# Kernel optimization log

Hardware: AMD Instinct MI355X
Metric: run time of the kernel (lower is better)

The kernel has to match this reference:

```python
import jax, jax.numpy as jnp
import numpy as np

DIM_X = 256
DIM_E = 256
SCALE = (DIM_X + DIM_E) ** -0.5


def setup_inputs() -> dict:
    key = jax.random.key(0)
    k1, k2, k3, k4 = jax.random.split(key, 4)
    b, n = 8, 2048
    d = DIM_X + DIM_E
    x = jax.random.normal(k1, (b, n, DIM_X), dtype=jnp.float32)
    e = jax.random.normal(k2, (n, DIM_E), dtype=jnp.float32)
    # nn.Linear(d, d, bias=False) weights, torch layout (out, in): y = x @ W.T
    Wq = jax.random.normal(k3, (d, d), dtype=jnp.float32) * 0.02
    Wk = jax.random.normal(k4, (d, d), dtype=jnp.float32) * 0.02
    return {"x": x, "e": e, "Wq": Wq, "Wk": Wk}


def reference(x, e, Wq, Wk):
    b, n, t = x.shape
    # e repeated across batch, concatenated with x along feature dim
    e_b = jnp.broadcast_to(e[None], (b, n, e.shape[-1]))
    x_e = jnp.concatenate([x, e_b], axis=-1)            # (b, n, dX+dE)
    queries = x_e @ Wq.T                                 # (b, n, d)
    keys = x_e @ Wk.T                                    # (b, n, d)
    # raw bilinear scores, no softmax; dropout=0 (eval) is identity
    attn = jnp.einsum('bnd,bmd->bnm', queries, keys) * SCALE
    out = jnp.einsum('bnm,bmt->bnt', attn, x)            # v = x
    return out
```

## Files before the change

kernel.cpp:

```cpp
#include <hip/hip_runtime.h>
#include <hip/hip_bf16.h>

#define DIM_X 256
#define DIM_E 256
#define DD    512
#define NB    8
#define NN    2048
#define SCALE 0.044194173824159216f

typedef __attribute__((ext_vector_type(8))) __bf16 bf16x8;
typedef __attribute__((ext_vector_type(4))) float  f32x4;
using bf16 = __hip_bfloat16;

__device__ __forceinline__ unsigned short f2bf(float f) {
  union { __hip_bfloat16 h; unsigned short u; } c;
  c.h = __float2bfloat16(f);
  return c.u;
}

__device__ __forceinline__ void async_lds16(const void* g, void* l) {
  using u32_as3 = __attribute__((address_space(3))) unsigned int;
  using u32_as1 = const __attribute__((address_space(1))) unsigned int;
  __builtin_amdgcn_global_load_lds(
      reinterpret_cast<u32_as1*>(reinterpret_cast<unsigned long long>(g)),
      reinterpret_cast<u32_as3*>(static_cast<unsigned int>(
          reinterpret_cast<unsigned long long>(l))),
      16, 0, 0);
}

__global__ __launch_bounds__(256, 4) void pack_k(
    const float* __restrict__ x, const float* __restrict__ e,
    const float* __restrict__ Wq, const float* __restrict__ Wk, bf16* xb,
    bf16* VT, bf16* eb, bf16* ET, bf16* WqT, bf16* WkT) {
  __shared__ float tile[32][33];
  const int tid  = threadIdx.x;
  const int lrow = tid >> 3;
  const int lc4  = (tid & 7) * 4;
  for (int j = blockIdx.x; j < 5120; j += 1024) {
    const float* src; int ld;
    bf16 *dS = nullptr, *dT; int ldS = 0, ldT;
    if (j < 4096) {
      int b = j >> 9, r = (j >> 3) & 63, c = j & 7;
      src = x + ((long)b * NN + r * 32) * DIM_X + c * 32; ld = DIM_X;
      dS = xb + ((long)b * NN + r * 32) * DIM_X + c * 32; ldS = DIM_X;
      dT = VT + ((long)b * DIM_X + c * 32) * NN + r * 32; ldT = NN;
    } else if (j < 4608) {
      int i = j - 4096, r = i >> 3, c = i & 7;
      src = e + ((long)r * 32) * DIM_E + c * 32; ld = DIM_E;
      dS = eb + ((long)r * 32) * DIM_E + c * 32; ldS = DIM_E;
      dT = ET + ((long)c * 32) * NN + r * 32; ldT = NN;
    } else if (j < 4864) {
      int i = j - 4608, r = i >> 4, c = i & 15;
      src = Wq + ((long)r * 32) * DD + c * 32; ld = DD;
      dT = WqT + ((long)c * 32) * DD + r * 32; ldT = DD;
    } else {
      int i = j - 4864, r = i >> 4, c = i & 15;
      src = Wk + ((long)r * 32) * DD + c * 32; ld = DD;
      dT = WkT + ((long)c * 32) * DD + r * 32; ldT = DD;
    }
    float4 v = *(const float4*)(src + (long)lrow * ld + lc4);
    if (dS) {
      ushort4 o;
      o.x = f2bf(v.x); o.y = f2bf(v.y); o.z = f2bf(v.z); o.w = f2bf(v.w);
      *(ushort4*)((unsigned short*)dS + (long)lrow * ldS + lc4) = o;
    }
    tile[lrow][lc4 + 0] = v.x; tile[lrow][lc4 + 1] = v.y;
    tile[lrow][lc4 + 2] = v.z; tile[lrow][lc4 + 3] = v.w;
    __syncthreads();
    {
      ushort4 o;
      o.x = f2bf(tile[lc4 + 0][lrow]);
      o.y = f2bf(tile[lc4 + 1][lrow]);
      o.z = f2bf(tile[lc4 + 2][lrow]);
      o.w = f2bf(tile[lc4 + 3][lrow]);
      *(ushort4*)((unsigned short*)dT + (long)lrow * ldT + lc4) = o;
    }
    __syncthreads();
  }
}

template <int BM, int BN, int BKt, bool OUT_BF16>
__device__ void gemm_tile(const bf16* __restrict__ A0,
                          const bf16* __restrict__ A1,
                          const bf16* __restrict__ B, void* __restrict__ Cv,
                          int K, int lda, int ldb, int ldc, float alpha,
                          char* smem) {
  constexpr int CPT = BKt / 8;
  constexpr int KS  = BKt / 32;
  constexpr int WTM = BM / 2, WTN = BN / 2;
  constexpr int IM = WTM / 16, IN = WTN / 16;
  constexpr int CA = BM * CPT, CB = BN * CPT;
  bf16* sA = (bf16*)smem;
  bf16* sB = (bf16*)(smem + (size_t)BM * BKt * 2);

  const int tid  = threadIdx.x;
  const int lane = tid & 63;
  const int wave = tid >> 6;
  const int lm   = lane & 15;
  const int quad = lane >> 4;
  const int wm   = (wave >> 1) * WTM;
  const int wn   = (wave & 1) * WTN;

  f32x4 acc[IM][IN];
#pragma unroll
  for (int i = 0; i < IM; i++)
#pragma unroll
    for (int j = 0; j < IN; j++) acc[i][j] = (f32x4){0.f, 0.f, 0.f, 0.f};

  for (int k0 = 0; k0 < K; k0 += BKt) {
    const bf16* Ak = A0; int kk = k0;
    if (A1 != nullptr && k0 >= 256) { Ak = A1; kk = k0 - 256; }
#pragma unroll
    for (int c = tid; c < CA; c += 256) {
      int row = c / CPT;
      int cb  = (c % CPT) ^ (row % CPT);
      async_lds16(Ak + (long)row * lda + kk + cb * 8, sA + (size_t)c * 8);
    }
#pragma unroll
    for (int c = tid; c < CB; c += 256) {
      int row = c / CPT;
      int cb  = (c % CPT) ^ (row % CPT);
      async_lds16(B + (long)row * ldb + k0 + cb * 8, sB + (size_t)c * 8);
    }
    __syncthreads();

    bf16x8 af[KS][IM], bfr[KS][IN];
#pragma unroll
    for (int s = 0; s < KS; s++) {
#pragma unroll
      for (int i = 0; i < IM; i++) {
        int r = wm + i * 16 + lm;
        af[s][i] = *(const bf16x8*)&sA[r * BKt +
                                       (((s * 4 + quad) ^ (r % CPT)) * 8)];
      }
#pragma unroll
      for (int j = 0; j < IN; j++) {
        int r = wn + j * 16 + lm;
        bfr[s][j] = *(const bf16x8*)&sB[r * BKt +
                                        (((s * 4 + quad) ^ (r % CPT)) * 8)];
      }
    }
#pragma unroll
    for (int s = 0; s < KS; s++)
#pragma unroll
      for (int i = 0; i < IM; i++)
#pragma unroll
        for (int j = 0; j < IN; j++)
          acc[i][j] = __builtin_amdgcn_mfma_f32_16x16x32_bf16(
              af[s][i], bfr[s][j], acc[i][j], 0, 0, 0);
    __syncthreads();
  }

  const int baseRow = wm + quad * 4;
  const int baseCol = wn + lm;
  if (OUT_BF16) {
    bf16* Cb = (bf16*)Cv;
#pragma unroll
    for (int i = 0; i < IM; i++)
#pragma unroll
      for (int r = 0; r < 4; r++) {
        int row = baseRow + i * 16 + r;
#pragma unroll
        for (int j = 0; j < IN; j++)
          Cb[(long)row * ldc + baseCol + j * 16] =
              __float2bfloat16(acc[i][j][r] * alpha);
      }
  } else {
    float* Cf = (float*)Cv;
#pragma unroll
    for (int i = 0; i < IM; i++)
#pragma unroll
      for (int r = 0; r < 4; r++) {
        int row = baseRow + i * 16 + r;
#pragma unroll
        for (int j = 0; j < IN; j++)
          Cf[(long)row * ldc + baseCol + j * 16] = acc[i][j][r] * alpha;
      }
  }
}

__global__ __launch_bounds__(256, 4) void phase1_k(const bf16* VT,
                                                   const bf16* ET,
                                                   const bf16* WqT,
                                                   const bf16* WkT, bf16* M,
                                                   bf16* W2T) {
  __shared__ __align__(16) char smem[32768];
  const int bx = blockIdx.x;
  if (bx < 512) {
    int b = bx & 7, r = (bx >> 3) & 7, c = bx >> 6;
    const bf16* A = VT + (long)b * DIM_X * NN + (long)r * 32 * NN;
    const bf16* B = (c < 4) ? VT + (long)b * DIM_X * NN + (long)c * 64 * NN
                            : ET + (long)(c - 4) * 64 * NN;
    gemm_tile<32, 64, 128, true>(
        A, nullptr, B, M + (long)b * DIM_X * DD + (long)r * 32 * DD + c * 64,
        NN, NN, NN, DD, 1.0f, smem);
  } else {
    int i = bx - 512, r2 = i >> 3, c2 = i & 7;
    gemm_tile<64, 64, 128, true>(WqT + (long)r2 * 64 * DD, nullptr,
                                 WkT + (long)c2 * 64 * DD,
                                 W2T + (long)r2 * 64 * DD + c2 * 64, DD, DD,
                                 DD, DD, 1.0f, smem);
  }
}

__global__ __launch_bounds__(256, 4) void phase2_k(const bf16* M,
                                                   const bf16* W2T, bf16* R) {
  __shared__ __align__(16) char smem[32768];
  const int bx = blockIdx.x;
  int b = bx & 7, r = (bx >> 3) & 7, c = bx >> 6;
  gemm_tile<32, 64, 128, true>(
      M + (long)b * DIM_X * DD + (long)r * 32 * DD, nullptr,
      W2T + (long)c * 64 * DD,
      R + (long)b * DIM_X * DD + (long)r * 32 * DD + c * 64, DD, DD, DD, DD,
      SCALE, smem);
}

__global__ __launch_bounds__(256, 3) void phase3_k(const bf16* xb,
                                                   const bf16* eb,
                                                   const bf16* R, float* out) {
  __shared__ __align__(16) char smem[49152];
  const int bx = blockIdx.x;
  int b = bx & 7, m = (bx >> 3) & 31, n = (bx >> 8) & 1;
  gemm_tile<64, 128, 128, false>(
      xb + (long)b * NN * DIM_X + (long)m * 64 * DIM_X,
      eb + (long)m * 64 * DIM_E,
      R + (long)b * DIM_X * DD + (long)n * 128 * DD,
      out + (long)b * NN * DIM_X + (long)m * 64 * DIM_X + n * 128, DD, DIM_X,
      DD, DIM_X, 1.0f, smem);
}


extern "C" void kernel_launch(void* const* d_in, const int* in_sizes, int n_in,
                              void* d_out, int out_size, void* d_ws,
                              size_t ws_size, hipStream_t stream) {
  const float* x  = (const float*)d_in[0];
  const float* e  = (const float*)d_in[1];
  const float* Wq = (const float*)d_in[2];
  const float* Wk = (const float*)d_in[3];
  float* out = (float*)d_out;

  char* ws = (char*)d_ws;
  size_t off = 0;
  auto alloc = [&](size_t bytes) {
    void* p = ws + off;
    off += (bytes + 255) & ~(size_t)255;
    return p;
  };

  bf16* xb  = (bf16*)alloc((size_t)NB * NN * DIM_X * 2);
  bf16* VT  = (bf16*)alloc((size_t)NB * DIM_X * NN * 2);
  bf16* eb  = (bf16*)alloc((size_t)NN * DIM_E * 2);
  bf16* ET  = (bf16*)alloc((size_t)DIM_E * NN * 2);
  bf16* WqT = (bf16*)alloc((size_t)DD * DD * 2);
  bf16* WkT = (bf16*)alloc((size_t)DD * DD * 2);
  bf16* W2T = (bf16*)alloc((size_t)DD * DD * 2);
  bf16* M   = (bf16*)alloc((size_t)NB * DIM_X * DD * 2);
  bf16* R   = (bf16*)alloc((size_t)NB * DIM_X * DD * 2);

  pack_k<<<1024, 256, 0, stream>>>(x, e, Wq, Wk, xb, VT, eb, ET, WqT, WkT);
  phase1_k<<<576, 256, 0, stream>>>(VT, ET, WqT, WkT, M, W2T);
  phase2_k<<<512, 256, 0, stream>>>(M, W2T, R);
  phase3_k<<<512, 256, 0, stream>>>(xb, eb, R, out);
}
```

Before: 105.5 us.

## Fuse four phases into one persistent kernel with software grid barriers

Replaces the four kernel launches (pack, phase1, phase2, phase3) with a single persistent kernel of 512 blocks separated by atomic sense-reversing grid barriers. Phase 1 is re-tiled to 64x64 with a split-K into two partial buffers (M1, M2), and phase 2 sums them by reading both halves along K, with the W2 product spread across a subset of blocks. The aim is to remove launch gaps and tail effects between phases. The risks are deadlock if not all 512 blocks are co-resident, barrier overhead, and lower occupancy from the 48KB shared allocation and launch bounds of 2.

```diff
diff --git a/kernel.cpp b/kernel.cpp
--- a/kernel.cpp
+++ b/kernel.cpp
@@ -7,6 +7,7 @@
 #define NB    8
 #define NN    2048
 #define SCALE 0.044194173824159216f
+#define GRID  512
 
 typedef __attribute__((ext_vector_type(8))) __bf16 bf16x8;
 typedef __attribute__((ext_vector_type(4))) float  f32x4;
@@ -28,61 +29,44 @@
       16, 0, 0);
 }
 
-__global__ __launch_bounds__(256, 4) void pack_k(
-    const float* __restrict__ x, const float* __restrict__ e,
-    const float* __restrict__ Wq, const float* __restrict__ Wk, bf16* xb,
-    bf16* VT, bf16* eb, bf16* ET, bf16* WqT, bf16* WkT) {
-  __shared__ float tile[32][33];
-  const int tid  = threadIdx.x;
-  const int lrow = tid >> 3;
-  const int lc4  = (tid & 7) * 4;
-  for (int j = blockIdx.x; j < 5120; j += 1024) {
-    const float* src; int ld;
-    bf16 *dS = nullptr, *dT; int ldS = 0, ldT;
-    if (j < 4096) {
-      int b = j >> 9, r = (j >> 3) & 63, c = j & 7;
-      src = x + ((long)b * NN + r * 32) * DIM_X + c * 32; ld = DIM_X;
-      dS = xb + ((long)b * NN + r * 32) * DIM_X + c * 32; ldS = DIM_X;
-      dT = VT + ((long)b * DIM_X + c * 32) * NN + r * 32; ldT = NN;
-    } else if (j < 4608) {
-      int i = j - 4096, r = i >> 3, c = i & 7;
-      src = e + ((long)r * 32) * DIM_E + c * 32; ld = DIM_E;
-      dS = eb + ((long)r * 32) * DIM_E + c * 32; ldS = DIM_E;
-      dT = ET + ((long)c * 32) * NN + r * 32; ldT = NN;
-    } else if (j < 4864) {
-      int i = j - 4608, r = i >> 4, c = i & 15;
-      src = Wq + ((long)r * 32) * DD + c * 32; ld = DD;
-      dT = WqT + ((long)c * 32) * DD + r * 32; ldT = DD;
+__device__ __align__(128) unsigned g_cnt   = 0u;
+__device__ __align__(128) unsigned g_sense = 0u;
+
+__device__ __forceinline__ void grid_sync() {
+  __syncthreads();
+  if (threadIdx.x == 0) {
+    unsigned s = __hip_atomic_load(&g_sense, __ATOMIC_RELAXED,
+                                   __HIP_MEMORY_SCOPE_AGENT);
+    unsigned prev = __hip_atomic_fetch_add(&g_cnt, 1u, __ATOMIC_ACQ_REL,
+                                           __HIP_MEMORY_SCOPE_AGENT);
+    if (prev == (unsigned)(GRID - 1)) {
+      __hip_atomic_store(&g_cnt, 0u, __ATOMIC_RELAXED,
+                         __HIP_MEMORY_SCOPE_AGENT);
+      __hip_atomic_store(&g_sense, s ^ 1u, __ATOMIC_RELEASE,
+                         __HIP_MEMORY_SCOPE_AGENT);
     } else {
-      int i = j - 4864, r = i >> 4, c = i & 15;
-      src = Wk + ((long)r * 32) * DD + c * 32; ld = DD;
-      dT = WkT + ((long)c * 32) * DD + r * 32; ldT = DD;
-    }
-    float4 v = *(const float4*)(src + (long)lrow * ld + lc4);
-    if (dS) {
-      ushort4 o;
-      o.x = f2bf(v.x); o.y = f2bf(v.y); o.z = f2bf(v.z); o.w = f2bf(v.w);
-      *(ushort4*)((unsigned short*)dS + (long)lrow * ldS + lc4) = o;
-    }
-    tile[lrow][lc4 + 0] = v.x; tile[lrow][lc4 + 1] = v.y;
-    tile[lrow][lc4 + 2] = v.z; tile[lrow][lc4 + 3] = v.w;
-    __syncthreads();
-    {
-      ushort4 o;
-      o.x = f2bf(tile[lc4 + 0][lrow]);
-      o.y = f2bf(tile[lc4 + 1][lrow]);
-      o.z = f2bf(tile[lc4 + 2][lrow]);
-      o.w = f2bf(tile[lc4 + 3][lrow]);
-      *(ushort4*)((unsigned short*)dT + (long)lrow * ldT + lc4) = o;
-    }
-    __syncthreads();
-  }
-}
-
-template <int BM, int BN, int BKt, bool OUT_BF16>
+      unsigned n = 0;
+      for (;;) {
+        unsigned v = ((++n) & 63u)
+                         ? __hip_atomic_load(&g_sense, __ATOMIC_RELAXED,
+                                             __HIP_MEMORY_SCOPE_AGENT)
+                         : __hip_atomic_fetch_add(&g_sense, 0u,
+                                                  __ATOMIC_RELAXED,
+                                                  __HIP_MEMORY_SCOPE_AGENT);
+        if (v != s) break;
+        __builtin_amdgcn_s_sleep(4);
+      }
+      __builtin_amdgcn_fence(__ATOMIC_ACQUIRE, "agent");
+    }
+  }
+  __syncthreads();
+}
+
+template <int BM, int BN, int BKt, bool OUT_BF16, int ASPLIT, int BSPLIT>
 __device__ void gemm_tile(const bf16* __restrict__ A0,
                           const bf16* __restrict__ A1,
-                          const bf16* __restrict__ B, void* __restrict__ Cv,
+                          const bf16* __restrict__ B0,
+                          const bf16* __restrict__ B1, void* __restrict__ Cv,
                           int K, int lda, int ldb, int ldc, float alpha,
                           char* smem) {
   constexpr int CPT = BKt / 8;
@@ -108,19 +92,21 @@
     for (int j = 0; j < IN; j++) acc[i][j] = (f32x4){0.f, 0.f, 0.f, 0.f};
 
   for (int k0 = 0; k0 < K; k0 += BKt) {
-    const bf16* Ak = A0; int kk = k0;
-    if (A1 != nullptr && k0 >= 256) { Ak = A1; kk = k0 - 256; }
+    const bf16* Ak = A0; int ka = k0;
+    if (ASPLIT > 0 && k0 >= ASPLIT) { Ak = A1; ka = k0 - ASPLIT; }
+    const bf16* Bk = B0; int kb = k0;
+    if (BSPLIT > 0 && k0 >= BSPLIT) { Bk = B1; kb = k0 - BSPLIT; }
 #pragma unroll
     for (int c = tid; c < CA; c += 256) {
       int row = c / CPT;
       int cb  = (c % CPT) ^ (row % CPT);
-      async_lds16(Ak + (long)row * lda + kk + cb * 8, sA + (size_t)c * 8);
+      async_lds16(Ak + (long)row * lda + ka + cb * 8, sA + (size_t)c * 8);
     }
 #pragma unroll
     for (int c = tid; c < CB; c += 256) {
       int row = c / CPT;
       int cb  = (c % CPT) ^ (row % CPT);
-      async_lds16(B + (long)row * ldb + k0 + cb * 8, sB + (size_t)c * 8);
+      async_lds16(Bk + (long)row * ldb + kb + cb * 8, sB + (size_t)c * 8);
     }
     __syncthreads();
 
@@ -179,54 +165,111 @@
   }
 }
 
-__global__ __launch_bounds__(256, 4) void phase1_k(const bf16* VT,
-                                                   const bf16* ET,
-                                                   const bf16* WqT,
-                                                   const bf16* WkT, bf16* M,
-                                                   bf16* W2T) {
-  __shared__ __align__(16) char smem[32768];
-  const int bx = blockIdx.x;
-  if (bx < 512) {
-    int b = bx & 7, r = (bx >> 3) & 7, c = bx >> 6;
-    const bf16* A = VT + (long)b * DIM_X * NN + (long)r * 32 * NN;
-    const bf16* B = (c < 4) ? VT + (long)b * DIM_X * NN + (long)c * 64 * NN
-                            : ET + (long)(c - 4) * 64 * NN;
-    gemm_tile<32, 64, 128, true>(
-        A, nullptr, B, M + (long)b * DIM_X * DD + (long)r * 32 * DD + c * 64,
-        NN, NN, NN, DD, 1.0f, smem);
-  } else {
-    int i = bx - 512, r2 = i >> 3, c2 = i & 7;
-    gemm_tile<64, 64, 128, true>(WqT + (long)r2 * 64 * DD, nullptr,
-                                 WkT + (long)c2 * 64 * DD,
-                                 W2T + (long)r2 * 64 * DD + c2 * 64, DD, DD,
-                                 DD, DD, 1.0f, smem);
-  }
-}
-
-__global__ __launch_bounds__(256, 4) void phase2_k(const bf16* M,
-                                                   const bf16* W2T, bf16* R) {
-  __shared__ __align__(16) char smem[32768];
-  const int bx = blockIdx.x;
-  int b = bx & 7, r = (bx >> 3) & 7, c = bx >> 6;
-  gemm_tile<32, 64, 128, true>(
-      M + (long)b * DIM_X * DD + (long)r * 32 * DD, nullptr,
-      W2T + (long)c * 64 * DD,
-      R + (long)b * DIM_X * DD + (long)r * 32 * DD + c * 64, DD, DD, DD, DD,
-      SCALE, smem);
-}
-
-__global__ __launch_bounds__(256, 3) void phase3_k(const bf16* xb,
-                                                   const bf16* eb,
-                                                   const bf16* R, float* out) {
+__global__ __launch_bounds__(256, 2) void fused_k(
+    const float* __restrict__ x, const float* __restrict__ e,
+    const float* __restrict__ Wq, const float* __restrict__ Wk,
+    bf16* __restrict__ xb, bf16* __restrict__ VT, bf16* __restrict__ eb,
+    bf16* __restrict__ ET, bf16* __restrict__ WqT, bf16* __restrict__ WkT,
+    bf16* __restrict__ W2T, bf16* __restrict__ M1, bf16* __restrict__ M2,
+    bf16* __restrict__ R, float* __restrict__ out) {
   __shared__ __align__(16) char smem[49152];
-  const int bx = blockIdx.x;
-  int b = bx & 7, m = (bx >> 3) & 31, n = (bx >> 8) & 1;
-  gemm_tile<64, 128, 128, false>(
-      xb + (long)b * NN * DIM_X + (long)m * 64 * DIM_X,
-      eb + (long)m * 64 * DIM_E,
-      R + (long)b * DIM_X * DD + (long)n * 128 * DD,
-      out + (long)b * NN * DIM_X + (long)m * 64 * DIM_X + n * 128, DD, DIM_X,
-      DD, DIM_X, 1.0f, smem);
+  const int bx  = blockIdx.x;
+  const int tid = threadIdx.x;
+
+  {
+    float (*tile)[33] = reinterpret_cast<float (*)[33]>(smem);
+    const int lrow = tid >> 3;
+    const int lc4  = (tid & 7) * 4;
+    for (int j = bx; j < 5120; j += GRID) {
+      const float* src; int ld;
+      bf16 *dS = nullptr, *dT; int ldS = 0, ldT;
+      if (j < 4096) {
+        int b = j >> 9, r = (j >> 3) & 63, c = j & 7;
+        src = x + ((long)b * NN + r * 32) * DIM_X + c * 32; ld = DIM_X;
+        dS = xb + ((long)b * NN + r * 32) * DIM_X + c * 32; ldS = DIM_X;
+        dT = VT + ((long)b * DIM_X + c * 32) * NN + r * 32; ldT = NN;
+      } else if (j < 4608) {
+        int i = j - 4096, r = i >> 3, c = i & 7;
+        src = e + ((long)r * 32) * DIM_E + c * 32; ld = DIM_E;
+        dS = eb + ((long)r * 32) * DIM_E + c * 32; ldS = DIM_E;
+        dT = ET + ((long)c * 32) * NN + r * 32; ldT = NN;
+      } else if (j < 4864) {
+        int i = j - 4608, r = i >> 4, c = i & 15;
+        src = Wq + ((long)r * 32) * DD + c * 32; ld = DD;
+        dT = WqT + ((long)c * 32) * DD + r * 32; ldT = DD;
+      } else {
+        int i = j - 4864, r = i >> 4, c = i & 15;
+        src = Wk + ((long)r * 32) * DD + c * 32; ld = DD;
+        dT = WkT + ((long)c * 32) * DD + r * 32; ldT = DD;
+      }
+      float4 v = *(const float4*)(src + (long)lrow * ld + lc4);
+      if (dS) {
+        ushort4 o;
+        o.x = f2bf(v.x); o.y = f2bf(v.y); o.z = f2bf(v.z); o.w = f2bf(v.w);
+        *(ushort4*)((unsigned short*)dS + (long)lrow * ldS + lc4) = o;
+      }
+      tile[lrow][lc4 + 0] = v.x; tile[lrow][lc4 + 1] = v.y;
+      tile[lrow][lc4 + 2] = v.z; tile[lrow][lc4 + 3] = v.w;
+      __syncthreads();
+      {
+        ushort4 o;
+        o.x = f2bf(tile[lc4 + 0][lrow]);
+        o.y = f2bf(tile[lc4 + 1][lrow]);
+        o.z = f2bf(tile[lc4 + 2][lrow]);
+        o.w = f2bf(tile[lc4 + 3][lrow]);
+        *(ushort4*)((unsigned short*)dT + (long)lrow * ldT + lc4) = o;
+      }
+      __syncthreads();
+    }
+  }
+  grid_sync();
+
+  {
+    const int b   = bx & 7;
+    const int idx = bx >> 3;
+    const int kh  = idx & 1;
+    const int mt  = (idx >> 1) & 3;
+    const int nt  = idx >> 3;
+    const bf16* A = VT + (long)b * DIM_X * NN + (long)mt * 64 * NN + kh * 1024;
+    const bf16* B = (nt < 4)
+        ? VT + (long)b * DIM_X * NN + (long)nt * 64 * NN + kh * 1024
+        : ET + (long)(nt - 4) * 64 * NN + kh * 1024;
+    bf16* C = (kh ? M2 : M1) + (long)b * DIM_X * DD + (long)mt * 64 * DD +
+              nt * 64;
+    gemm_tile<64, 64, 128, true, 0, 0>(A, nullptr, B, nullptr, C, 1024, NN,
+                                       NN, DD, 1.0f, smem);
+    const int k = bx >> 3;
+    if ((bx & 7) == (k & 7)) {
+      int r2 = k >> 3, c2 = k & 7;
+      gemm_tile<64, 64, 128, true, 0, 0>(
+          WqT + (long)r2 * 64 * DD, nullptr, WkT + (long)c2 * 64 * DD,
+          nullptr, W2T + (long)r2 * 64 * DD + c2 * 64, DD, DD, DD, DD, 1.0f,
+          smem);
+    }
+  }
+  grid_sync();
+
+  {
+    const int b = bx & 7, r = (bx >> 3) & 7, c = bx >> 6;
+    const bf16* a0 = M1 + (long)b * DIM_X * DD + (long)r * 32 * DD;
+    const bf16* a1 = M2 + (long)b * DIM_X * DD + (long)r * 32 * DD;
+    const bf16* w  = W2T + (long)c * 64 * DD;
+    gemm_tile<32, 64, 128, true, 512, 512>(
+        a0, a1, w, w,
+        R + (long)b * DIM_X * DD + (long)r * 32 * DD + c * 64, 1024, DD, DD,
+        DD, SCALE, smem);
+  }
+  grid_sync();
+
+  {
+    const int b = bx & 7, m = (bx >> 3) & 31, n = (bx >> 8) & 1;
+    gemm_tile<64, 128, 128, false, 256, 0>(
+        xb + (long)b * NN * DIM_X + (long)m * 64 * DIM_X,
+        eb + (long)m * 64 * DIM_E,
+        R + (long)b * DIM_X * DD + (long)n * 128 * DD, nullptr,
+        out + (long)b * NN * DIM_X + (long)m * 64 * DIM_X + n * 128, DD,
+        DIM_X, DD, DIM_X, 1.0f, smem);
+  }
 }
 
 
@@ -254,11 +297,10 @@
   bf16* WqT = (bf16*)alloc((size_t)DD * DD * 2);
   bf16* WkT = (bf16*)alloc((size_t)DD * DD * 2);
   bf16* W2T = (bf16*)alloc((size_t)DD * DD * 2);
-  bf16* M   = (bf16*)alloc((size_t)NB * DIM_X * DD * 2);
+  bf16* M1  = (bf16*)alloc((size_t)NB * DIM_X * DD * 2);
+  bf16* M2  = (bf16*)alloc((size_t)NB * DIM_X * DD * 2);
   bf16* R   = (bf16*)alloc((size_t)NB * DIM_X * DD * 2);
 
-  pack_k<<<1024, 256, 0, stream>>>(x, e, Wq, Wk, xb, VT, eb, ET, WqT, WkT);
-  phase1_k<<<576, 256, 0, stream>>>(VT, ET, WqT, WkT, M, W2T);
-  phase2_k<<<512, 256, 0, stream>>>(M, W2T, R);
-  phase3_k<<<512, 256, 0, stream>>>(xb, eb, R, out);
-}
+  fused_k<<<GRID, 256, 0, stream>>>(x, e, Wq, Wk, xb, VT, eb, ET, WqT, WkT,
+                                    W2T, M1, M2, R, out);
+}
```

After: 165.6 us. 57.0% more time.

## Double-buffer GEMM tiles, split-K phase1, one tile per pack block

Applied to the files above, without the earlier changes.

Adds double-buffered LDS staging to the shared GEMM tile so the next K-slice's async global-to-LDS loads overlap the current slice's MFMA work. Phase1's Gram-matrix GEMM is split into two K halves with 64x64 tiles written to separate buffers M1/M2. Phase2 sums the halves by running a K=1024 GEMM over the concatenated M1/M2 against a repeated W2T. The pack kernel now launches one block per tile instead of grid-striding, and tile K depths are changed. This trades extra workspace and an extra partial-sum write/read for better latency hiding and more parallel blocks.

```diff
diff --git a/kernel.cpp b/kernel.cpp
--- a/kernel.cpp
+++ b/kernel.cpp
@@ -36,62 +36,60 @@
   const int tid  = threadIdx.x;
   const int lrow = tid >> 3;
   const int lc4  = (tid & 7) * 4;
-  for (int j = blockIdx.x; j < 5120; j += 1024) {
-    const float* src; int ld;
-    bf16 *dS = nullptr, *dT; int ldS = 0, ldT;
-    if (j < 4096) {
-      int b = j >> 9, r = (j >> 3) & 63, c = j & 7;
-      src = x + ((long)b * NN + r * 32) * DIM_X + c * 32; ld = DIM_X;
-      dS = xb + ((long)b * NN + r * 32) * DIM_X + c * 32; ldS = DIM_X;
-      dT = VT + ((long)b * DIM_X + c * 32) * NN + r * 32; ldT = NN;
-    } else if (j < 4608) {
-      int i = j - 4096, r = i >> 3, c = i & 7;
-      src = e + ((long)r * 32) * DIM_E + c * 32; ld = DIM_E;
-      dS = eb + ((long)r * 32) * DIM_E + c * 32; ldS = DIM_E;
-      dT = ET + ((long)c * 32) * NN + r * 32; ldT = NN;
-    } else if (j < 4864) {
-      int i = j - 4608, r = i >> 4, c = i & 15;
-      src = Wq + ((long)r * 32) * DD + c * 32; ld = DD;
-      dT = WqT + ((long)c * 32) * DD + r * 32; ldT = DD;
-    } else {
-      int i = j - 4864, r = i >> 4, c = i & 15;
-      src = Wk + ((long)r * 32) * DD + c * 32; ld = DD;
-      dT = WkT + ((long)c * 32) * DD + r * 32; ldT = DD;
-    }
-    float4 v = *(const float4*)(src + (long)lrow * ld + lc4);
-    if (dS) {
-      ushort4 o;
-      o.x = f2bf(v.x); o.y = f2bf(v.y); o.z = f2bf(v.z); o.w = f2bf(v.w);
-      *(ushort4*)((unsigned short*)dS + (long)lrow * ldS + lc4) = o;
-    }
-    tile[lrow][lc4 + 0] = v.x; tile[lrow][lc4 + 1] = v.y;
-    tile[lrow][lc4 + 2] = v.z; tile[lrow][lc4 + 3] = v.w;
-    __syncthreads();
-    {
-      ushort4 o;
-      o.x = f2bf(tile[lc4 + 0][lrow]);
-      o.y = f2bf(tile[lc4 + 1][lrow]);
-      o.z = f2bf(tile[lc4 + 2][lrow]);
-      o.w = f2bf(tile[lc4 + 3][lrow]);
-      *(ushort4*)((unsigned short*)dT + (long)lrow * ldT + lc4) = o;
-    }
-    __syncthreads();
-  }
-}
-
-template <int BM, int BN, int BKt, bool OUT_BF16>
+  const int j    = blockIdx.x;
+  const float* src; int ld;
+  bf16 *dS = nullptr, *dT; int ldS = 0, ldT;
+  if (j < 4096) {
+    int b = j >> 9, r = (j >> 3) & 63, c = j & 7;
+    src = x + ((long)b * NN + r * 32) * DIM_X + c * 32; ld = DIM_X;
+    dS = xb + ((long)b * NN + r * 32) * DIM_X + c * 32; ldS = DIM_X;
+    dT = VT + ((long)b * DIM_X + c * 32) * NN + r * 32; ldT = NN;
+  } else if (j < 4608) {
+    int i = j - 4096, r = i >> 3, c = i & 7;
+    src = e + ((long)r * 32) * DIM_E + c * 32; ld = DIM_E;
+    dS = eb + ((long)r * 32) * DIM_E + c * 32; ldS = DIM_E;
+    dT = ET + ((long)c * 32) * NN + r * 32; ldT = NN;
+  } else if (j < 4864) {
+    int i = j - 4608, r = i >> 4, c = i & 15;
+    src = Wq + ((long)r * 32) * DD + c * 32; ld = DD;
+    dT = WqT + ((long)c * 32) * DD + r * 32; ldT = DD;
+  } else {
+    int i = j - 4864, r = i >> 4, c = i & 15;
+    src = Wk + ((long)r * 32) * DD + c * 32; ld = DD;
+    dT = WkT + ((long)c * 32) * DD + r * 32; ldT = DD;
+  }
+  float4 v = *(const float4*)(src + (long)lrow * ld + lc4);
+  if (dS) {
+    ushort4 o;
+    o.x = f2bf(v.x); o.y = f2bf(v.y); o.z = f2bf(v.z); o.w = f2bf(v.w);
+    *(ushort4*)((unsigned short*)dS + (long)lrow * ldS + lc4) = o;
+  }
+  tile[lrow][lc4 + 0] = v.x; tile[lrow][lc4 + 1] = v.y;
+  tile[lrow][lc4 + 2] = v.z; tile[lrow][lc4 + 3] = v.w;
+  __syncthreads();
+  {
+    ushort4 o;
+    o.x = f2bf(tile[lc4 + 0][lrow]);
+    o.y = f2bf(tile[lc4 + 1][lrow]);
+    o.z = f2bf(tile[lc4 + 2][lrow]);
+    o.w = f2bf(tile[lc4 + 3][lrow]);
+    *(ushort4*)((unsigned short*)dT + (long)lrow * ldT + lc4) = o;
+  }
+}
+
+template <int BM, int BN, int BKt, bool OUT_BF16, int ASPLIT, int BSPLIT>
 __device__ void gemm_tile(const bf16* __restrict__ A0,
                           const bf16* __restrict__ A1,
-                          const bf16* __restrict__ B, void* __restrict__ Cv,
+                          const bf16* __restrict__ B0,
+                          const bf16* __restrict__ B1, void* __restrict__ Cv,
                           int K, int lda, int ldb, int ldc, float alpha,
                           char* smem) {
-  constexpr int CPT = BKt / 8;
-  constexpr int KS  = BKt / 32;
-  constexpr int WTM = BM / 2, WTN = BN / 2;
-  constexpr int IM = WTM / 16, IN = WTN / 16;
-  constexpr int CA = BM * CPT, CB = BN * CPT;
-  bf16* sA = (bf16*)smem;
-  bf16* sB = (bf16*)(smem + (size_t)BM * BKt * 2);
+  constexpr int CPT  = BKt / 8;
+  constexpr int KS   = BKt / 32;
+  constexpr int WTM  = BM / 2, WTN = BN / 2;
+  constexpr int IM   = WTM / 16, IN = WTN / 16;
+  constexpr int CA   = BM * CPT, CB = BN * CPT;
+  constexpr int BUFB = (BM + BN) * BKt * 2;
 
   const int tid  = threadIdx.x;
   const int lane = tid & 63;
@@ -101,29 +99,42 @@
   const int wm   = (wave >> 1) * WTM;
   const int wn   = (wave & 1) * WTN;
 
-  f32x4 acc[IM][IN];
-#pragma unroll
-  for (int i = 0; i < IM; i++)
-#pragma unroll
-    for (int j = 0; j < IN; j++) acc[i][j] = (f32x4){0.f, 0.f, 0.f, 0.f};
-
-  for (int k0 = 0; k0 < K; k0 += BKt) {
-    const bf16* Ak = A0; int kk = k0;
-    if (A1 != nullptr && k0 >= 256) { Ak = A1; kk = k0 - 256; }
+  auto stage = [&](int t, int buf) {
+    const int k0 = t * BKt;
+    const bf16* Ak = A0; int ka = k0;
+    if (ASPLIT > 0 && k0 >= ASPLIT) { Ak = A1; ka = k0 - ASPLIT; }
+    const bf16* Bk = B0; int kb = k0;
+    if (BSPLIT > 0 && k0 >= BSPLIT) { Bk = B1; kb = k0 - BSPLIT; }
+    bf16* sA = (bf16*)(smem + (size_t)buf * BUFB);
+    bf16* sB = sA + BM * BKt;
 #pragma unroll
     for (int c = tid; c < CA; c += 256) {
       int row = c / CPT;
       int cb  = (c % CPT) ^ (row % CPT);
-      async_lds16(Ak + (long)row * lda + kk + cb * 8, sA + (size_t)c * 8);
+      async_lds16(Ak + (long)row * lda + ka + cb * 8, sA + (size_t)c * 8);
     }
 #pragma unroll
     for (int c = tid; c < CB; c += 256) {
       int row = c / CPT;
       int cb  = (c % CPT) ^ (row % CPT);
-      async_lds16(B + (long)row * ldb + k0 + cb * 8, sB + (size_t)c * 8);
+      async_lds16(Bk + (long)row * ldb + kb + cb * 8, sB + (size_t)c * 8);
     }
-    __syncthreads();
-
+  };
+
+  f32x4 acc[IM][IN];
+#pragma unroll
+  for (int i = 0; i < IM; i++)
+#pragma unroll
+    for (int j = 0; j < IN; j++) acc[i][j] = (f32x4){0.f, 0.f, 0.f, 0.f};
+
+  const int nt = K / BKt;
+  stage(0, 0);
+  __syncthreads();
+  int cur = 0;
+  for (int t = 0; t < nt; ++t) {
+    if (t + 1 < nt) stage(t + 1, cur ^ 1);
+    const bf16* sA = (const bf16*)(smem + (size_t)cur * BUFB);
+    const bf16* sB = sA + BM * BKt;
     bf16x8 af[KS][IM], bfr[KS][IN];
 #pragma unroll
     for (int s = 0; s < KS; s++) {
@@ -149,6 +160,7 @@
           acc[i][j] = __builtin_amdgcn_mfma_f32_16x16x32_bf16(
               af[s][i], bfr[s][j], acc[i][j], 0, 0, 0);
     __syncthreads();
+    cur ^= 1;
   }
 
   const int baseRow = wm + quad * 4;
@@ -179,40 +191,46 @@
   }
 }
 
-__global__ __launch_bounds__(256, 4) void phase1_k(const bf16* VT,
-                                                   const bf16* ET,
-                                                   const bf16* WqT,
-                                                   const bf16* WkT, bf16* M,
-                                                   bf16* W2T) {
+__global__ __launch_bounds__(256, 4) void phase1_k(
+    const bf16* VT, const bf16* ET, const bf16* WqT, const bf16* WkT,
+    bf16* M1, bf16* M2, bf16* W2T) {
   __shared__ __align__(16) char smem[32768];
   const int bx = blockIdx.x;
-  if (bx < 512) {
-    int b = bx & 7, r = (bx >> 3) & 7, c = bx >> 6;
-    const bf16* A = VT + (long)b * DIM_X * NN + (long)r * 32 * NN;
-    const bf16* B = (c < 4) ? VT + (long)b * DIM_X * NN + (long)c * 64 * NN
-                            : ET + (long)(c - 4) * 64 * NN;
-    gemm_tile<32, 64, 128, true>(
-        A, nullptr, B, M + (long)b * DIM_X * DD + (long)r * 32 * DD + c * 64,
-        NN, NN, NN, DD, 1.0f, smem);
+  if (bx < 64) {
+    int r2 = bx >> 3, c2 = bx & 7;
+    gemm_tile<64, 64, 64, true, 0, 0>(
+        WqT + (long)r2 * 64 * DD, nullptr, WkT + (long)c2 * 64 * DD, nullptr,
+        W2T + (long)r2 * 64 * DD + c2 * 64, DD, DD, DD, DD, 1.0f, smem);
   } else {
-    int i = bx - 512, r2 = i >> 3, c2 = i & 7;
-    gemm_tile<64, 64, 128, true>(WqT + (long)r2 * 64 * DD, nullptr,
-                                 WkT + (long)c2 * 64 * DD,
-                                 W2T + (long)r2 * 64 * DD + c2 * 64, DD, DD,
-                                 DD, DD, 1.0f, smem);
-  }
-}
-
-__global__ __launch_bounds__(256, 4) void phase2_k(const bf16* M,
+    const int j   = bx - 64;
+    const int b   = j & 7;
+    const int idx = j >> 3;
+    const int kh  = idx & 1;
+    const int mt  = (idx >> 1) & 3;
+    const int nt  = idx >> 3;
+    const bf16* A = VT + (long)b * DIM_X * NN + (long)mt * 64 * NN + kh * 1024;
+    const bf16* B = (nt < 4)
+        ? VT + (long)b * DIM_X * NN + (long)nt * 64 * NN + kh * 1024
+        : ET + (long)(nt - 4) * 64 * NN + kh * 1024;
+    bf16* C = (kh ? M2 : M1) + (long)b * DIM_X * DD + (long)mt * 64 * DD +
+              nt * 64;
+    gemm_tile<64, 64, 64, true, 0, 0>(A, nullptr, B, nullptr, C, 1024, NN,
+                                      NN, DD, 1.0f, smem);
+  }
+}
+
+__global__ __launch_bounds__(256, 3) void phase2_k(const bf16* M1,
+                                                   const bf16* M2,
                                                    const bf16* W2T, bf16* R) {
-  __shared__ __align__(16) char smem[32768];
+  __shared__ __align__(16) char smem[49152];
   const int bx = blockIdx.x;
-  int b = bx & 7, r = (bx >> 3) & 7, c = bx >> 6;
-  gemm_tile<32, 64, 128, true>(
-      M + (long)b * DIM_X * DD + (long)r * 32 * DD, nullptr,
-      W2T + (long)c * 64 * DD,
-      R + (long)b * DIM_X * DD + (long)r * 32 * DD + c * 64, DD, DD, DD, DD,
-      SCALE, smem);
+  const int b = bx & 7, r = (bx >> 3) & 7, c = bx >> 6;
+  const bf16* a0 = M1 + (long)b * DIM_X * DD + (long)r * 32 * DD;
+  const bf16* a1 = M2 + (long)b * DIM_X * DD + (long)r * 32 * DD;
+  const bf16* w  = W2T + (long)c * 64 * DD;
+  gemm_tile<32, 64, 128, true, 512, 512>(
+      a0, a1, w, w, R + (long)b * DIM_X * DD + (long)r * 32 * DD + c * 64,
+      1024, DD, DD, DD, SCALE, smem);
 }
 
 __global__ __launch_bounds__(256, 3) void phase3_k(const bf16* xb,
@@ -220,11 +238,11 @@
                                                    const bf16* R, float* out) {
   __shared__ __align__(16) char smem[49152];
   const int bx = blockIdx.x;
-  int b = bx & 7, m = (bx >> 3) & 31, n = (bx >> 8) & 1;
-  gemm_tile<64, 128, 128, false>(
+  const int b = bx & 7, m = (bx >> 3) & 31, n = (bx >> 8) & 1;
+  gemm_tile<64, 128, 64, false, 256, 0>(
       xb + (long)b * NN * DIM_X + (long)m * 64 * DIM_X,
       eb + (long)m * 64 * DIM_E,
-      R + (long)b * DIM_X * DD + (long)n * 128 * DD,
+      R + (long)b * DIM_X * DD + (long)n * 128 * DD, nullptr,
       out + (long)b * NN * DIM_X + (long)m * 64 * DIM_X + n * 128, DD, DIM_X,
       DD, DIM_X, 1.0f, smem);
 }
@@ -254,11 +272,12 @@
   bf16* WqT = (bf16*)alloc((size_t)DD * DD * 2);
   bf16* WkT = (bf16*)alloc((size_t)DD * DD * 2);
   bf16* W2T = (bf16*)alloc((size_t)DD * DD * 2);
-  bf16* M   = (bf16*)alloc((size_t)NB * DIM_X * DD * 2);
+  bf16* M1  = (bf16*)alloc((size_t)NB * DIM_X * DD * 2);
+  bf16* M2  = (bf16*)alloc((size_t)NB * DIM_X * DD * 2);
   bf16* R   = (bf16*)alloc((size_t)NB * DIM_X * DD * 2);
 
-  pack_k<<<1024, 256, 0, stream>>>(x, e, Wq, Wk, xb, VT, eb, ET, WqT, WkT);
-  phase1_k<<<576, 256, 0, stream>>>(VT, ET, WqT, WkT, M, W2T);
-  phase2_k<<<512, 256, 0, stream>>>(M, W2T, R);
+  pack_k<<<5120, 256, 0, stream>>>(x, e, Wq, Wk, xb, VT, eb, ET, WqT, WkT);
+  phase1_k<<<576, 256, 0, stream>>>(VT, ET, WqT, WkT, M1, M2, W2T);
+  phase2_k<<<512, 256, 0, stream>>>(M1, M2, W2T, R);
   phase3_k<<<512, 256, 0, stream>>>(xb, eb, R, out);
 }
```

After: 106.0 us. About the same (+0.5%).
